# Performance work log

Measured on AMD Instinct MI355X. Metric: run time of the kernel, lower is better.

The kernel has to match this reference:

```python
import jax, jax.numpy as jnp
import numpy as np

N = 50000   # nodes
E = 600000  # edges
IN = 512    # in_channels
H = 128     # hidden_channels
B = 64      # graphs in batch
L = 4       # GatedGraphConv layers
VIEWS = [[0, 9, 10], [1, 2, 3], [4, 5, 6], [7, 8, 11, 12]]  # syntactic/sequential/semantic/discourse


def layer_norm(x, w, b, eps=1e-5):
    mu = x.mean(-1, keepdims=True)
    var = ((x - mu) ** 2).mean(-1, keepdims=True)
    return (x - mu) / jnp.sqrt(var + eps) * w + b


def setup_inputs() -> dict:
    key = jax.random.key(0)
    ks = jax.random.split(key, 32)
    p = lambda k, shape: (jax.random.normal(k, shape, jnp.float32) * 0.02)
    inp = {
        'x': jax.random.normal(ks[0], (N, IN), jnp.float32),
        'edge_index': jax.random.randint(ks[1], (2, E), 0, N, dtype=jnp.int32),
        'edge_type': jax.random.randint(ks[2], (E,), 0, 13, dtype=jnp.int32),
        'batch': jnp.sort(jax.random.randint(ks[3], (N,), 0, B, dtype=jnp.int32)),
        # input projection (Linear + LayerNorm)
        'proj_w': p(ks[4], (IN, H)), 'proj_b': p(ks[5], (H,)),
        'ln0_w': jnp.ones((H,), jnp.float32), 'ln0_b': jnp.zeros((H,), jnp.float32),
        # per-view GatedGraphConv: weight [views, layers, H, H] + GRUCell params [views, 3H, H]
        'ggnn_w': p(ks[6], (4, L, H, H)),
        'gru_wih': p(ks[7], (4, 3 * H, H)), 'gru_whh': p(ks[8], (4, 3 * H, H)),
        'gru_bih': p(ks[9], (4, 3 * H)), 'gru_bhh': p(ks[10], (4, 3 * H)),
        # per-view LayerNorm
        'vln_w': jnp.ones((4, H), jnp.float32), 'vln_b': jnp.zeros((4, H), jnp.float32),
        # attention fusion
        'q_w': p(ks[11], (H, H)), 'q_b': p(ks[12], (H,)),
        'k_w': p(ks[13], (H, H)), 'k_b': p(ks[14], (H,)),
        # classifier MLP: 2H -> H -> H//2 -> 1
        'c1_w': p(ks[15], (2 * H, H)), 'c1_b': p(ks[16], (H,)),
        'c2_w': p(ks[17], (H, H // 2)), 'c2_b': p(ks[18], (H // 2,)),
        'c3_w': p(ks[19], (H // 2, 1)), 'c3_b': p(ks[20], (1,)),
    }
    return inp


def reference(x, edge_index, edge_type, batch, proj_w, proj_b, ln0_w, ln0_b,
              ggnn_w, gru_wih, gru_whh, gru_bih, gru_bhh, vln_w, vln_b,
              q_w, q_b, k_w, k_b, c1_w, c1_b, c2_w, c2_b, c3_w, c3_b):
    # input projection: Linear -> LayerNorm -> GELU (dropout = identity in eval)
    h0 = jax.nn.gelu(layer_norm(x @ proj_w + proj_b, ln0_w, ln0_b), approximate=False)
    src, dst = edge_index[0], edge_index[1]
    views = []
    for v in range(4):
        emask = jnp.zeros((E,), bool)
        for t in VIEWS[v]:
            emask = emask | (edge_type == t)
        em = emask.astype(h0.dtype)[:, None]  # [E,1] edge-type view mask
        h = h0
        for i in range(L):
            m = h @ ggnn_w[v, i]                                   # [N,H]
            agg = jax.ops.segment_sum(m[src] * em, dst, num_segments=N)  # masked scatter-add
            # GRUCell(input=agg, hidden=h), torch gate order r,z,n
            gi = agg @ gru_wih[v].T + gru_bih[v]
            gh = h @ gru_whh[v].T + gru_bhh[v]
            ir, iz, inn = jnp.split(gi, 3, -1)
            hr, hz, hn = jnp.split(gh, 3, -1)
            r = jax.nn.sigmoid(ir + hr)
            z = jax.nn.sigmoid(iz + hz)
            n = jnp.tanh(inn + r * hn)
            h = (1.0 - z) * n + z * h
        views.append(layer_norm(h, vln_w[v], vln_b[v]) + h0)  # residual ViewEncoder
    hs = jnp.stack(views, 1)  # [N,4,H]
    # node-conditioned attention fusion
    q = jnp.tanh(h0 @ q_w + q_b)
    keys = hs @ k_w + k_b
    attn = jax.nn.softmax(jnp.einsum('nh,nvh->nv', q, keys) * (H ** -0.5), axis=-1)
    fused = jnp.einsum('nvh,nv->nh', hs, attn)
    # global mean + max pooling per graph
    cnt = jax.ops.segment_sum(jnp.ones((N,), fused.dtype), batch, num_segments=B)
    x_mean = jax.ops.segment_sum(fused, batch, num_segments=B) / jnp.maximum(cnt, 1.0)[:, None]
    x_max = jax.ops.segment_max(fused, batch, num_segments=B)
    g = jnp.concatenate([x_mean, x_max], -1)  # [B,2H]
    h1 = jax.nn.relu(g @ c1_w + c1_b)
    h2 = jax.nn.relu(h1 @ c2_w + c2_b)
    return h2 @ c3_w + c3_b  # [B,1] logits
```

## Files before the change

### kernel.cpp

```cpp
#include <hip/hip_runtime.h>
#include <math.h>


typedef __attribute__((ext_vector_type(8))) short short8;
typedef __attribute__((ext_vector_type(4))) float floatx4;

__device__ __forceinline__ unsigned short f2bf_rtn(float x) {
    unsigned u = __float_as_uint(x);
    return (unsigned short)((u + 0x7FFFu + ((u >> 16) & 1u)) >> 16);
}
__device__ __forceinline__ float bf2f(unsigned short h) {
    return __uint_as_float((unsigned)h << 16);
}
__device__ __forceinline__ float fsig(float x) {
    return __builtin_amdgcn_rcpf(1.0f + __expf(-x));
}
__device__ __forceinline__ float ftanh(float x) {
    return 1.0f - 2.0f * __builtin_amdgcn_rcpf(__expf(2.0f * x) + 1.0f);
}

__device__ __forceinline__ int view_of(int t) {
    return (t >= 1 && t <= 3) ? 1 : (t >= 4 && t <= 6) ? 2
         : ((t == 7) || (t == 8) || (t >= 11)) ? 3 : 0;
}

template <bool BT, int EPI>
__global__ __launch_bounds__(256, 2) void gemm_k(
    const float* __restrict__ A, const float* __restrict__ Bm,
    const float* __restrict__ bias, float* __restrict__ C,
    int N, int M, int K, long sA, long sB, long sC)
{
    __shared__ float As[32][132];
    __shared__ float Bs[32][132];
    A  += (long)blockIdx.z * sA;
    Bm += (long)blockIdx.z * sB;
    C  += (long)blockIdx.z * sC;
    const int r0 = blockIdx.x * 128;
    const int c0 = blockIdx.y * 128;
    const int tid = threadIdx.x;
    const int tx = tid & 15;
    const int ty = tid >> 4;

    float acc[8][8];
#pragma unroll
    for (int i = 0; i < 8; i++)
#pragma unroll
        for (int j = 0; j < 8; j++) acc[i][j] = 0.0f;

    for (int k0 = 0; k0 < K; k0 += 32) {
        {
            int arow = tid >> 3;
            int akq  = (tid & 7) << 2;
#pragma unroll
            for (int hh = 0; hh < 4; hh++) {
                int r  = arow + hh * 32;
                int gr = r0 + r;
                float4 av = make_float4(0.f, 0.f, 0.f, 0.f);
                if (gr < N) av = *(const float4*)(A + (long)gr * K + k0 + akq);
                As[akq + 0][r] = av.x; As[akq + 1][r] = av.y;
                As[akq + 2][r] = av.z; As[akq + 3][r] = av.w;
            }
        }
        if (BT) {
            int brow = tid >> 3;
            int bkq  = (tid & 7) << 2;
#pragma unroll
            for (int hh = 0; hh < 4; hh++) {
                int r = brow + hh * 32;
                float4 bv = *(const float4*)(Bm + (long)(c0 + r) * K + k0 + bkq);
                Bs[bkq + 0][r] = bv.x; Bs[bkq + 1][r] = bv.y;
                Bs[bkq + 2][r] = bv.z; Bs[bkq + 3][r] = bv.w;
            }
        } else {
            int kk0 = tid >> 5;
            int bmq = (tid & 31) << 2;
#pragma unroll
            for (int hh = 0; hh < 4; hh++) {
                int kk = kk0 + hh * 8;
                float4 bv = *(const float4*)(Bm + (long)(k0 + kk) * M + c0 + bmq);
                *(float4*)&Bs[kk][bmq] = bv;
            }
        }
        __syncthreads();
#pragma unroll
        for (int k = 0; k < 32; k++) {
            float4 a0 = *(const float4*)&As[k][ty << 2];
            float4 a1 = *(const float4*)&As[k][64 + (ty << 2)];
            float4 b0 = *(const float4*)&Bs[k][tx << 2];
            float4 b1 = *(const float4*)&Bs[k][64 + (tx << 2)];
            float av[8] = {a0.x, a0.y, a0.z, a0.w, a1.x, a1.y, a1.z, a1.w};
            float bv[8] = {b0.x, b0.y, b0.z, b0.w, b1.x, b1.y, b1.z, b1.w};
#pragma unroll
            for (int i = 0; i < 8; i++)
#pragma unroll
                for (int j = 0; j < 8; j++) acc[i][j] += av[i] * bv[j];
        }
        __syncthreads();
    }

    float bb[8] = {0, 0, 0, 0, 0, 0, 0, 0};
    if (bias) {
        float4 b0 = *(const float4*)(bias + c0 + (tx << 2));
        float4 b1 = *(const float4*)(bias + c0 + 64 + (tx << 2));
        bb[0] = b0.x; bb[1] = b0.y; bb[2] = b0.z; bb[3] = b0.w;
        bb[4] = b1.x; bb[5] = b1.y; bb[6] = b1.z; bb[7] = b1.w;
    }
#pragma unroll
    for (int i = 0; i < 8; i++) {
        int r = (i < 4) ? (r0 + (ty << 2) + i) : (r0 + 64 + (ty << 2) + i - 4);
        if (r < N) {
            float v[8];
#pragma unroll
            for (int j = 0; j < 8; j++) {
                v[j] = acc[i][j] + bb[j];
                if (EPI == 1) v[j] = tanhf(v[j]);
            }
            *(float4*)(C + (long)r * M + c0 + (tx << 2)) = make_float4(v[0], v[1], v[2], v[3]);
            *(float4*)(C + (long)r * M + c0 + 64 + (tx << 2)) = make_float4(v[4], v[5], v[6], v[7]);
        }
    }
}

__global__ __launch_bounds__(256) void build_p_k(
    const float* __restrict__ gwih, const float* __restrict__ gwhh,
    const float* __restrict__ gbih, const float* __restrict__ gbhh,
    float* __restrict__ pih, float* __restrict__ phh, float* __restrict__ bp)
{
    int idx = blockIdx.x * 256 + threadIdx.x;
    if (idx < 16 * 65536) {
        int z = idx >> 16, rem = idx & 65535;
        int k = rem >> 9, mcol = rem & 511;
        int ch = mcol >> 2, g = mcol & 3;
        int v = z >> 2;
        const float* Wih = gwih + (long)v * 384 * 128;
        float val = 0.0f;
        if (g == 0) val = Wih[ch * 128 + k];
        else if (g == 1) val = Wih[(128 + ch) * 128 + k];
        else if (g == 2) val = Wih[(256 + ch) * 128 + k];
        pih[idx] = val;
    }
    if (idx < 4 * 65536) {
        int v = idx >> 16, rem = idx & 65535;
        int k = rem >> 9, mcol = rem & 511;
        int ch = mcol >> 2, g = mcol & 3;
        const float* Whh = gwhh + (long)v * 384 * 128;
        float val = 0.0f;
        if (g == 0) val = Whh[ch * 128 + k];
        else if (g == 1) val = Whh[(128 + ch) * 128 + k];
        else if (g == 3) val = Whh[(256 + ch) * 128 + k];
        phh[idx] = val;
    }
    if (idx < 4 * 512) {
        int v = idx >> 9, mcol = idx & 511;
        int ch = mcol >> 2, g = mcol & 3;
        float val;
        if (g == 0) val = gbih[v * 384 + ch] + gbhh[v * 384 + ch];
        else if (g == 1) val = gbih[v * 384 + 128 + ch] + gbhh[v * 384 + 128 + ch];
        else if (g == 2) val = gbih[v * 384 + 256 + ch];
        else val = gbhh[v * 384 + 256 + ch];
        bp[idx] = val;
    }
}

__global__ __launch_bounds__(256) void pack_b_k(
    const float* __restrict__ wcomb, const float* __restrict__ phh,
    short* __restrict__ Bp)
{
    int idx = blockIdx.x * 256 + threadIdx.x;
    if (idx >= 16 * 256 * 512) return;
    int z = idx >> 17, rem = idx & 131071;
    int k = rem >> 9, col = rem & 511;
    int g  = col & 3;
    int q  = (col >> 2) & 3;
    int tn = (col >> 4) & 7;
    int ch = ((col >> 7) << 5) + (q << 3) + tn;
    int mcol = (ch << 2) + g;
    float val = (k < 128) ? wcomb[(long)z * 65536 + k * 512 + mcol]
                          : phh[(long)(z >> 2) * 65536 + (k - 128) * 512 + mcol];
    long dst = ((long)(z * 8 + (k >> 5)) * 512 + col) * 32 + ((k >> 3) & 3) * 8 + (k & 7);
    Bp[dst] = (short)f2bf_rtn(val);
}

template <bool BT>
__global__ __launch_bounds__(256) void pack_w_k(
    const float* __restrict__ W, short* __restrict__ bhi, short* __restrict__ blo, int K)
{
    int idx = blockIdx.x * 256 + threadIdx.x;
    if (idx >= K * 128) return;
    int k = idx >> 7, col = idx & 127;
    float v = BT ? W[col * K + k] : W[k * 128 + col];
    unsigned short h = f2bf_rtn(v);
    float fh = __uint_as_float((unsigned)h << 16);
    long dst = ((long)(k >> 5) * 128 + col) * 32 + ((k >> 3) & 3) * 8 + (k & 7);
    bhi[dst] = (short)h;
    blo[dst] = (short)f2bf_rtn(v - fh);
}

template <int EPI>
__global__ __launch_bounds__(256, 4) void gemm_mfma_k(
    const float* __restrict__ A, const short* __restrict__ Bhi,
    const short* __restrict__ Blo, const float* __restrict__ bias,
    float* __restrict__ C, int N, int K)
{
    __shared__ __align__(16) short Ahi[64 * 40];
    __shared__ __align__(16) short Alo[64 * 40];
    const int r0 = blockIdx.x * 64;
    const int tid = threadIdx.x;
    const int l = tid & 63, w = tid >> 6;
    const int wrow = w * 16;
    const int m = l & 15, q = l >> 4;

    floatx4 acc[8];
#pragma unroll
    for (int b = 0; b < 8; b++) acc[b] = (floatx4)0.0f;

    const int arow = tid >> 2;
    const int fcol = (tid & 3) * 8;
    const int gr = r0 + arow;
    const int nks = K >> 5;

    for (int ks = 0; ks < nks; ks++) {
        float xv[8];
        if (gr < N) {
            float4 x0 = *(const float4*)(A + (long)gr * K + ks * 32 + fcol);
            float4 x1 = *(const float4*)(A + (long)gr * K + ks * 32 + fcol + 4);
            xv[0] = x0.x; xv[1] = x0.y; xv[2] = x0.z; xv[3] = x0.w;
            xv[4] = x1.x; xv[5] = x1.y; xv[6] = x1.z; xv[7] = x1.w;
        } else {
#pragma unroll
            for (int u = 0; u < 8; u++) xv[u] = 0.0f;
        }
        short8 vhi, vlo;
#pragma unroll
        for (int u = 0; u < 8; u++) {
            unsigned short hb = f2bf_rtn(xv[u]);
            float fh = __uint_as_float((unsigned)hb << 16);
            vhi[u] = (short)hb;
            vlo[u] = (short)f2bf_rtn(xv[u] - fh);
        }
        *(short8*)&Ahi[arow * 40 + fcol] = vhi;
        *(short8*)&Alo[arow * 40 + fcol] = vlo;
        __syncthreads();
        short8 ah = *(short8*)&Ahi[(wrow + m) * 40 + q * 8];
        short8 al = *(short8*)&Alo[(wrow + m) * 40 + q * 8];
#pragma unroll
        for (int tn = 0; tn < 8; tn++) {
            int col = tn * 16 + m;
            short8 bh = *(const short8*)(Bhi + ((long)ks * 128 + col) * 32 + q * 8);
            short8 bl = *(const short8*)(Blo + ((long)ks * 128 + col) * 32 + q * 8);
            acc[tn] = __builtin_amdgcn_mfma_f32_16x16x32_bf16(ah, bh, acc[tn], 0, 0, 0);
            acc[tn] = __builtin_amdgcn_mfma_f32_16x16x32_bf16(al, bh, acc[tn], 0, 0, 0);
            acc[tn] = __builtin_amdgcn_mfma_f32_16x16x32_bf16(ah, bl, acc[tn], 0, 0, 0);
        }
        __syncthreads();
    }

#pragma unroll
    for (int tn = 0; tn < 8; tn++) {
        int col = tn * 16 + m;
        float bb = bias ? bias[col] : 0.0f;
#pragma unroll
        for (int reg = 0; reg < 4; reg++) {
            int row = r0 + wrow + q * 4 + reg;
            if (row < N) {
                float v = acc[tn][reg] + bb;
                if (EPI == 1) v = ftanh(v);
                C[(long)row * 128 + col] = v;
            }
        }
    }
}

__global__ __launch_bounds__(256, 4) void gemm_gru_mfma_k(
    const short* __restrict__ hb, const short* __restrict__ hpHi,
    const short* __restrict__ hpLo, const short* __restrict__ Bp,
    const float* __restrict__ bp, short* __restrict__ outHi,
    short* __restrict__ outLo, const int* __restrict__ off,
    const int* __restrict__ esrc, int N, long sV, long sHb, long sHp)
{
    __shared__ __align__(16) short As[8 * 64 * 40];
    const int xb = blockIdx.x;
    const int x = (xb & 7) | ((xb >> 4) << 3);
    const int yb = (xb >> 3) & 1;
    if (x * 64 >= N) return;
    const int z = blockIdx.z;
    const short* hbz = hb + (long)z * sHb;
    const short* hph = hpHi + (long)z * sHp;
    const short* hpl = hpLo + (long)z * sHp;
    Bp  += (long)z * 524288;
    bp  += (long)z * 512;
    outHi += (long)z * sV;
    outLo += (long)z * sV;
    const int r0  = x * 64;
    const int c0b = yb * 256;
    const int tid = threadIdx.x;
    const int l = tid & 63, w = tid >> 6;
    const int wrow = (w & 1) * 32, wcol = (w >> 1) * 128;
    const int m = l & 15, q = l >> 4;

    const int arow = tid >> 2;
    const int fcol = (tid & 3) * 8;
    const int gr = r0 + arow;

    {
        const int cg = tid & 3;
        float accS[32];
#pragma unroll
        for (int u = 0; u < 32; u++) accS[u] = 0.0f;
        if (gr < N) {
            const int idx = z * N + gr;
            int j = off[idx];
            const int end = off[idx + 1];
            if (j < end) {
                const short* sp = hb + (long)esrc[j] * 128 + (cg << 5);
                short8 p0 = *(const short8*)(sp);
                short8 p1 = *(const short8*)(sp + 8);
                short8 p2 = *(const short8*)(sp + 16);
                short8 p3 = *(const short8*)(sp + 24);
                for (; j < end;) {
                    short8 c0 = p0, c1 = p1, c2 = p2, c3 = p3;
                    ++j;
                    if (j < end) {
                        const short* sq = hb + (long)esrc[j] * 128 + (cg << 5);
                        p0 = *(const short8*)(sq);
                        p1 = *(const short8*)(sq + 8);
                        p2 = *(const short8*)(sq + 16);
                        p3 = *(const short8*)(sq + 24);
                    }
#pragma unroll
                    for (int u = 0; u < 8; u++) {
                        accS[u]      += bf2f((unsigned short)c0[u]);
                        accS[8 + u]  += bf2f((unsigned short)c1[u]);
                        accS[16 + u] += bf2f((unsigned short)c2[u]);
                        accS[24 + u] += bf2f((unsigned short)c3[u]);
                    }
                }
            }
        }
#pragma unroll
        for (int ub = 0; ub < 4; ub++) {
            short8 o;
#pragma unroll
            for (int u = 0; u < 8; u++) o[u] = (short)f2bf_rtn(accS[ub * 8 + u]);
            *(short8*)&As[cg * 2560 + arow * 40 + ub * 8] = o;
        }
    }

#pragma unroll
    for (int ks2 = 0; ks2 < 4; ks2++) {
        short8 av = (short8)0;
        if (gr < N) av = *(const short8*)(hbz + (long)gr * 128 + ks2 * 32 + fcol);
        *(short8*)&As[(4 + ks2) * 2560 + arow * 40 + fcol] = av;
    }
    __syncthreads();

    floatx4 acc[2][8];
#pragma unroll
    for (int a = 0; a < 2; a++)
#pragma unroll
        for (int b = 0; b < 8; b++) acc[a][b] = (floatx4)0.0f;

#pragma unroll
    for (int ks = 0; ks < 8; ks++) {
        short8 bfr[8];
#pragma unroll
        for (int tn = 0; tn < 8; tn++) {
            int col = c0b + wcol + tn * 16 + m;
            bfr[tn] = *(const short8*)(Bp + ((long)ks * 512 + col) * 32 + q * 8);
        }
        short8 a0 = *(short8*)&As[ks * 2560 + (wrow + m) * 40 + q * 8];
        short8 a1 = *(short8*)&As[ks * 2560 + (wrow + 16 + m) * 40 + q * 8];
#pragma unroll
        for (int tn = 0; tn < 8; tn++) {
            acc[0][tn] = __builtin_amdgcn_mfma_f32_16x16x32_bf16(bfr[tn], a0, acc[0][tn], 0, 0, 0);
            acc[1][tn] = __builtin_amdgcn_mfma_f32_16x16x32_bf16(bfr[tn], a1, acc[1][tn], 0, 0, 0);
        }
    }

    const int chq = ((c0b + wcol) >> 2) + q * 8;
#pragma unroll
    for (int a = 0; a < 2; a++) {
        const int row = r0 + wrow + a * 16 + m;
        if (row < N) {
            short8 h8 = *(const short8*)(hph + (long)row * 128 + chq);
            short8 l8 = *(const short8*)(hpl + (long)row * 128 + chq);
            float hnv[8];
            short8 ohi, olo;
#pragma unroll
            for (int tn = 0; tn < 8; tn++) {
                float hp = bf2f((unsigned short)h8[tn]) + bf2f((unsigned short)l8[tn]);
                float4 bv = *(const float4*)(bp + (chq + tn) * 4);
                floatx4 A = acc[a][tn];
                float rr = fsig(A[0] + bv.x);
                float zz = fsig(A[1] + bv.y);
                float nn = ftanh(A[2] + bv.z + rr * (A[3] + bv.w));
                hnv[tn] = (1.0f - zz) * nn + zz * hp;
                unsigned short hh = f2bf_rtn(hnv[tn]);
                ohi[tn] = (short)hh;
                olo[tn] = (short)f2bf_rtn(hnv[tn] - bf2f(hh));
            }
            *(short8*)(outHi + (long)row * 128 + chq) = ohi;
            *(short8*)(outLo + (long)row * 128 + chq) = olo;
        }
    }
}

__global__ __launch_bounds__(256) void ln_gelu_k(
    float* __restrict__ h0, short* __restrict__ h0b, short* __restrict__ h0lo,
    const float* __restrict__ w, const float* __restrict__ b, int N)
{
    long t = (long)blockIdx.x * 256 + threadIdx.x;
    int n = (int)(t >> 5), lane = (int)(t & 31);
    if (n >= N) return;
    float* p = h0 + (long)n * 128 + lane * 4;
    float4 x = *(float4*)p;
    float s = x.x + x.y + x.z + x.w;
#pragma unroll
    for (int off = 16; off >= 1; off >>= 1) s += __shfl_xor(s, off);
    float mu = s * (1.0f / 128.0f);
    float4 d = make_float4(x.x - mu, x.y - mu, x.z - mu, x.w - mu);
    float ss = d.x * d.x + d.y * d.y + d.z * d.z + d.w * d.w;
#pragma unroll
    for (int off = 16; off >= 1; off >>= 1) ss += __shfl_xor(ss, off);
    float inv = 1.0f / sqrtf(ss * (1.0f / 128.0f) + 1e-5f);
    float4 wv = *(const float4*)(w + lane * 4);
    float4 bv = *(const float4*)(b + lane * 4);
    float y[4] = {d.x * inv * wv.x + bv.x, d.y * inv * wv.y + bv.y,
                  d.z * inv * wv.z + bv.z, d.w * inv * wv.w + bv.w};
#pragma unroll
    for (int i = 0; i < 4; i++)
        y[i] = 0.5f * y[i] * (1.0f + erff(y[i] * 0.70710678118654752f));
    *(float4*)p = make_float4(y[0], y[1], y[2], y[3]);
    ushort4 hb, lb;
    hb.x = f2bf_rtn(y[0]); lb.x = f2bf_rtn(y[0] - bf2f(hb.x));
    hb.y = f2bf_rtn(y[1]); lb.y = f2bf_rtn(y[1] - bf2f(hb.y));
    hb.z = f2bf_rtn(y[2]); lb.z = f2bf_rtn(y[2] - bf2f(hb.z));
    hb.w = f2bf_rtn(y[3]); lb.w = f2bf_rtn(y[3] - bf2f(hb.w));
    *(ushort4*)(h0b + (long)n * 128 + lane * 4) = hb;
    *(ushort4*)(h0lo + (long)n * 128 + lane * 4) = lb;
}

__global__ __launch_bounds__(256) void count_k(
    const int* __restrict__ dst, const int* __restrict__ et,
    int* __restrict__ cnt, int E, int N)
{
    int e = blockIdx.x * 256 + threadIdx.x;
    if (e >= E) return;
    int v = view_of(et[e]);
    atomicAdd(&cnt[v * N + dst[e]], 1);
}

__global__ __launch_bounds__(256) void scan1_k(
    const int* __restrict__ cnt, int* __restrict__ off, int* __restrict__ bsum, int n)
{
    __shared__ int sm[256];
    int base = blockIdx.x * 1024;
    int tid = threadIdx.x;
    int v[4]; int s = 0;
#pragma unroll
    for (int i = 0; i < 4; i++) {
        int idx = base + tid * 4 + i;
        v[i] = (idx < n) ? cnt[idx] : 0; s += v[i];
    }
    sm[tid] = s; __syncthreads();
    for (int o = 1; o < 256; o <<= 1) {
        int t2 = (tid >= o) ? sm[tid - o] : 0;
        __syncthreads(); sm[tid] += t2; __syncthreads();
    }
    int run = sm[tid] - s;
    if (tid == 255) bsum[blockIdx.x] = sm[255];
#pragma unroll
    for (int i = 0; i < 4; i++) {
        int idx = base + tid * 4 + i;
        if (idx < n) off[idx] = run;
        run += v[i];
    }
}

__global__ __launch_bounds__(256) void scan2_k(int* __restrict__ bsum, int nb)
{
    __shared__ int sm[256];
    int tid = threadIdx.x;
    int v = (tid < nb) ? bsum[tid] : 0;
    sm[tid] = v; __syncthreads();
    for (int o = 1; o < 256; o <<= 1) {
        int t2 = (tid >= o) ? sm[tid - o] : 0;
        __syncthreads(); sm[tid] += t2; __syncthreads();
    }
    if (tid < nb) bsum[tid] = sm[tid] - v;
}

__global__ __launch_bounds__(256) void scan3_k(
    int* __restrict__ off, int* __restrict__ cursor,
    const int* __restrict__ bsum, int n, int total)
{
    int i = blockIdx.x * 256 + threadIdx.x;
    if (i < n) {
        int o = off[i] + bsum[i >> 10];
        off[i] = o; cursor[i] = o;
    }
    if (i == 0) off[n] = total;
}

__global__ __launch_bounds__(256) void fill_k(
    const int* __restrict__ src, const int* __restrict__ dst,
    const int* __restrict__ et, int* __restrict__ cursor,
    int* __restrict__ esrc, int* __restrict__ esrc0, int E, int N)
{
    int e = blockIdx.x * 256 + threadIdx.x;
    if (e >= E) return;
    int v = view_of(et[e]);
    int b = v * N + dst[e];
    int pos = atomicAdd(&cursor[b], 1);
    esrc[pos] = v * N + src[e];
    esrc0[pos] = src[e];
}

__global__ __launch_bounds__(256) void fusion_k(
    const short* __restrict__ hi, const short* __restrict__ lo,
    const float* __restrict__ h0, const float* __restrict__ q,
    const float* __restrict__ u, const float* __restrict__ kb,
    const float* __restrict__ vw, const float* __restrict__ vb,
    float* __restrict__ fused, int N)
{
    long t = (long)blockIdx.x * 256 + threadIdx.x;
    int n = (int)(t >> 5), lane = (int)(t & 31);
    if (n >= N) return;
    float4 qv = *(const float4*)(q + (long)n * 128 + lane * 4);
    float4 kv = *(const float4*)(kb + lane * 4);
    float4 uv = *(const float4*)(u + (long)n * 128 + lane * 4);
    float4 h0v = *(const float4*)(h0 + (long)n * 128 + lane * 4);
    float part = qv.x * kv.x + qv.y * kv.y + qv.z * kv.z + qv.w * kv.w;
    float hs[4][4];
    float lg[4];
#pragma unroll
    for (int v = 0; v < 4; v++) {
        long base = ((long)v * N + n) * 128 + lane * 4;
        ushort4 hu = *(const ushort4*)(hi + base);
        ushort4 lu = *(const ushort4*)(lo + base);
        float hv0 = bf2f(hu.x) + bf2f(lu.x);
        float hv1 = bf2f(hu.y) + bf2f(lu.y);
        float hv2 = bf2f(hu.z) + bf2f(lu.z);
        float hv3 = bf2f(hu.w) + bf2f(lu.w);
        float s = hv0 + hv1 + hv2 + hv3;
#pragma unroll
        for (int off = 16; off >= 1; off >>= 1) s += __shfl_xor(s, off);
        float mu = s * (1.0f / 128.0f);
        float d0 = hv0 - mu, d1 = hv1 - mu, d2 = hv2 - mu, d3 = hv3 - mu;
        float ss = d0 * d0 + d1 * d1 + d2 * d2 + d3 * d3;
#pragma unroll
        for (int off = 16; off >= 1; off >>= 1) ss += __shfl_xor(ss, off);
        float inv = 1.0f / sqrtf(ss * (1.0f / 128.0f) + 1e-5f);
        float4 wv = *(const float4*)(vw + v * 128 + lane * 4);
        float4 bv = *(const float4*)(vb + v * 128 + lane * 4);
        hs[v][0] = d0 * inv * wv.x + bv.x + h0v.x;
        hs[v][1] = d1 * inv * wv.y + bv.y + h0v.y;
        hs[v][2] = d2 * inv * wv.z + bv.z + h0v.z;
        hs[v][3] = d3 * inv * wv.w + bv.w + h0v.w;
        lg[v] = hs[v][0] * uv.x + hs[v][1] * uv.y + hs[v][2] * uv.z + hs[v][3] * uv.w;
    }
#pragma unroll
    for (int off = 16; off >= 1; off >>= 1) {
        part += __shfl_xor(part, off);
#pragma unroll
        for (int v = 0; v < 4; v++) lg[v] += __shfl_xor(lg[v], off);
    }
    const float scale = 0.08838834764831845f;
    float mx = -1e30f;
#pragma unroll
    for (int v = 0; v < 4; v++) { lg[v] = (lg[v] + part) * scale; mx = fmaxf(mx, lg[v]); }
    float se = 0.0f;
#pragma unroll
    for (int v = 0; v < 4; v++) { lg[v] = expf(lg[v] - mx); se += lg[v]; }
    float inv = 1.0f / se;
    float4 f = make_float4(0.f, 0.f, 0.f, 0.f);
#pragma unroll
    for (int v = 0; v < 4; v++) {
        float a = lg[v] * inv;
        f.x += a * hs[v][0]; f.y += a * hs[v][1];
        f.z += a * hs[v][2]; f.w += a * hs[v][3];
    }
    *(float4*)(fused + (long)n * 128 + lane * 4) = f;
}

__global__ __launch_bounds__(256) void pool_k(
    const float* __restrict__ fused, const int* __restrict__ batch,
    float* __restrict__ meanb, float* __restrict__ maxb, int N)
{
    __shared__ float s_sum[256], s_max[256];
    int b = blockIdx.x;
    int lo = 0, hi = N;
    while (lo < hi) { int mid = (lo + hi) >> 1; if (batch[mid] < b) lo = mid + 1; else hi = mid; }
    int beg = lo;
    lo = beg; hi = N;
    while (lo < hi) { int mid = (lo + hi) >> 1; if (batch[mid] < b + 1) lo = mid + 1; else hi = mid; }
    int end = lo;
    int tid = threadIdx.x;
    int c = tid & 127, half = tid >> 7;
    float sum = 0.0f, mx = __int_as_float(0xff800000);
    for (int n = beg + half; n < end; n += 2) {
        float v = fused[(long)n * 128 + c];
        sum += v; mx = fmaxf(mx, v);
    }
    s_sum[tid] = sum; s_max[tid] = mx;
    __syncthreads();
    if (half == 0) {
        float tot = s_sum[tid] + s_sum[tid + 128];
        float m2 = fmaxf(s_max[tid], s_max[tid + 128]);
        int cnt = end - beg;
        meanb[b * 128 + c] = tot / (float)max(cnt, 1);
        maxb[b * 128 + c] = m2;
    }
}

__global__ __launch_bounds__(256) void classifier_k(
    const float* __restrict__ meanb, const float* __restrict__ maxb,
    const float* __restrict__ c1w, const float* __restrict__ c1b,
    const float* __restrict__ c2w, const float* __restrict__ c2b,
    const float* __restrict__ c3w, const float* __restrict__ c3b,
    float* __restrict__ out)
{
    __shared__ float g[256];
    __shared__ float h1[128];
    __shared__ float h2[64];
    int b = blockIdx.x, tid = threadIdx.x;
    g[tid] = (tid < 128) ? meanb[b * 128 + tid] : maxb[b * 128 + (tid - 128)];
    __syncthreads();
    if (tid < 128) {
        float acc = c1b[tid];
        for (int k = 0; k < 256; k++) acc += g[k] * c1w[k * 128 + tid];
        h1[tid] = fmaxf(acc, 0.0f);
    }
    __syncthreads();
    if (tid < 64) {
        float acc = c2b[tid];
        for (int k = 0; k < 128; k++) acc += h1[k] * c2w[k * 64 + tid];
        h2[tid] = fmaxf(acc, 0.0f);
    }
    __syncthreads();
    if (tid < 64) {
        float p = h2[tid] * c3w[tid];
#pragma unroll
        for (int off = 32; off >= 1; off >>= 1) p += __shfl_xor(p, off);
        if (tid == 0) out[b] = c3b[0] + p;
    }
}

extern "C" void kernel_launch(void* const* d_in, const int* in_sizes, int n_in,
                              void* d_out, int out_size, void* d_ws, size_t ws_size,
                              hipStream_t stream) {
    (void)n_in; (void)out_size; (void)ws_size;
    const float* x      = (const float*)d_in[0];
    const int*   eidx   = (const int*)d_in[1];
    const int*   etype  = (const int*)d_in[2];
    const int*   batch  = (const int*)d_in[3];
    const float* proj_w = (const float*)d_in[4];
    const float* proj_b = (const float*)d_in[5];
    const float* ln0_w  = (const float*)d_in[6];
    const float* ln0_b  = (const float*)d_in[7];
    const float* ggnn_w = (const float*)d_in[8];
    const float* gwih   = (const float*)d_in[9];
    const float* gwhh   = (const float*)d_in[10];
    const float* gbih   = (const float*)d_in[11];
    const float* gbhh   = (const float*)d_in[12];
    const float* vln_w  = (const float*)d_in[13];
    const float* vln_b  = (const float*)d_in[14];
    const float* q_w    = (const float*)d_in[15];
    const float* q_b    = (const float*)d_in[16];
    const float* k_w    = (const float*)d_in[17];
    const float* k_b    = (const float*)d_in[18];
    const float* c1w    = (const float*)d_in[19];
    const float* c1b    = (const float*)d_in[20];
    const float* c2w    = (const float*)d_in[21];
    const float* c2b    = (const float*)d_in[22];
    const float* c3w    = (const float*)d_in[23];
    const float* c3b    = (const float*)d_in[24];
    float* out = (float*)d_out;

    const int N = in_sizes[3];
    const int E = in_sizes[2];
    const int IN = in_sizes[0] / N;
    const int H = 128, L = 4;
    const int N4 = 4 * N;

    long NH = (long)N * H;
    float* ws = (float*)d_ws;
    float* h0 = ws;
    float* hfz = h0 + NH;
    short* loA = (short*)hfz;
    short* loB = loA + 4 * NH;
    float* poolMean = hfz + 4 * NH;
    float* poolMax  = poolMean + 8192;
    float* bp = poolMax + 8192;
    short* h0b = (short*)(bp + 2048);
    short* hiA = h0b + NH;
    short* hiB = hiA + 4 * NH;
    short* Sb  = hiB + 4 * NH;
    short* Bp  = Sb + 4 * NH;
    short* prjHi = Bp + 16 * 131072;
    short* prjLo = prjHi + 65536;
    short* qwHi  = prjLo + 65536;
    short* qwLo  = qwHi + 16384;
    short* kwHi  = qwLo + 16384;
    short* kwLo  = kwHi + 16384;
    int* iOff  = (int*)(kwLo + 16384);
    int* iCnt  = iOff + N4 + 1;
    int* iCur  = iCnt + N4;
    int* iBsum = iCur + N4;
    int* iEsrc  = iBsum + 256;
    int* iEsrc0 = iEsrc + E;
    float* wcomb = hfz;
    float* pih   = hfz + 16 * 65536;
    float* phh   = pih + 16 * 65536;
    short* lo0 = loB;
    float* qbuf  = (float*)Sb;
    float* ubuf  = qbuf + NH;
    float* fused = (float*)hiA;

    int rb = (int)(((long)N * 32 + 255) / 256);
    int eb = (E + 255) / 256;
    int nbScan = (N4 + 1023) / 1024;
    int gx64 = (N + 63) / 64;
    int gxp = ((gx64 + 7) / 8) * 8;

    const int* esrc_in = eidx;
    const int* edst_in = eidx + E;

    hipMemsetAsync(iCnt, 0, (size_t)N4 * sizeof(int), stream);
    count_k<<<eb, 256, 0, stream>>>(edst_in, etype, iCnt, E, N);
    scan1_k<<<nbScan, 256, 0, stream>>>(iCnt, iOff, iBsum, N4);
    scan2_k<<<1, 256, 0, stream>>>(iBsum, nbScan);
    scan3_k<<<(N4 + 255) / 256, 256, 0, stream>>>(iOff, iCur, iBsum, N4, E);
    fill_k<<<eb, 256, 0, stream>>>(esrc_in, edst_in, etype, iCur, iEsrc, iEsrc0, E, N);

    build_p_k<<<(16 * 65536 + 255) / 256, 256, 0, stream>>>(
        gwih, gwhh, gbih, gbhh, pih, phh, bp);
    gemm_k<false, 0><<<dim3(1, 4, 16), 256, 0, stream>>>(
        ggnn_w, pih, nullptr, wcomb, 128, 512, 128,
        (long)H * H, 65536, 65536);
    pack_b_k<<<(16 * 256 * 512 + 255) / 256, 256, 0, stream>>>(wcomb, phh, Bp);
    pack_w_k<false><<<(IN * 128 + 255) / 256, 256, 0, stream>>>(proj_w, prjHi, prjLo, IN);
    pack_w_k<false><<<(128 * 128 + 255) / 256, 256, 0, stream>>>(q_w, qwHi, qwLo, 128);
    pack_w_k<true><<<(128 * 128 + 255) / 256, 256, 0, stream>>>(k_w, kwHi, kwLo, 128);

    gemm_mfma_k<0><<<gx64, 256, 0, stream>>>(x, prjHi, prjLo, proj_b, h0, N, IN);
    ln_gelu_k<<<rb, 256, 0, stream>>>(h0, h0b, lo0, ln0_w, ln0_b, N);

    const short* hin = h0b;  long sHb = 0;
    const short* hpH = h0b;  const short* hpL = lo0;  long sHp = 0;
    short* oHi = hiA; short* oLo = loA;
    for (int i = 0; i < L; i++) {
        const int* es = (i == 0) ? iEsrc0 : iEsrc;
        gemm_gru_mfma_k<<<dim3(2 * gxp, 1, 4), 256, 0, stream>>>(
            hin, hpH, hpL, Bp + (long)i * 131072, bp, oHi, oLo, iOff, es,
            N, NH, sHb, sHp);
        hpH = oHi; hpL = oLo; sHp = NH;
        hin = oHi; sHb = NH;
        if (oHi == hiA) { oHi = hiB; oLo = loB; }
        else            { oHi = hiA; oLo = loA; }
    }

    gemm_mfma_k<1><<<gx64, 256, 0, stream>>>(h0, qwHi, qwLo, q_b, qbuf, N, 128);
    gemm_mfma_k<0><<<gx64, 256, 0, stream>>>(qbuf, kwHi, kwLo, nullptr, ubuf, N, 128);
    fusion_k<<<rb, 256, 0, stream>>>(hiB, loB, h0, qbuf, ubuf, k_b,
                                     vln_w, vln_b, fused, N);
    pool_k<<<64, 256, 0, stream>>>(fused, batch, poolMean, poolMax, N);
    classifier_k<<<64, 256, 0, stream>>>(
        poolMean, poolMax, c1w, c1b, c2w, c2b, c3w, c3b, out);
}
```

Measured before the change: 1.286 ms.

## Merge GRU gemm column halves into one 512-thread block per row tile

The fused gather+GEMM+GRU kernel previously launched two 256-thread blocks per 64-row tile, one for each half of the 512 gate columns, and each block repeated the neighbour aggregation for the same rows. Now a single 512-thread block covers all 512 columns: eight waves tile the output, and the gather is spread over eight threads per row with half the accumulator registers each. This removes the duplicated irregular gather work and the swizzled block indexing. In exchange, launch bounds move to 512 threads with a higher occupancy target, which tightens the per-thread register budget for the MFMA accumulators and may cause spills.

New measurement: 2.167 ms. +68.5%, slower.

```diff
diff --git a/kernel.cpp b/kernel.cpp
--- a/kernel.cpp
+++ b/kernel.cpp
@@ -271,7 +271,7 @@
     }
 }
 
-__global__ __launch_bounds__(256, 4) void gemm_gru_mfma_k(
+__global__ __launch_bounds__(512, 6) void gemm_gru_mfma_k(
     const short* __restrict__ hb, const short* __restrict__ hpHi,
     const short* __restrict__ hpLo, const short* __restrict__ Bp,
     const float* __restrict__ bp, short* __restrict__ outHi,
@@ -279,10 +279,7 @@
     const int* __restrict__ esrc, int N, long sV, long sHb, long sHp)
 {
     __shared__ __align__(16) short As[8 * 64 * 40];
-    const int xb = blockIdx.x;
-    const int x = (xb & 7) | ((xb >> 4) << 3);
-    const int yb = (xb >> 3) & 1;
-    if (x * 64 >= N) return;
+    const int x = blockIdx.x;
     const int z = blockIdx.z;
     const short* hbz = hb + (long)z * sHb;
     const short* hph = hpHi + (long)z * sHp;
@@ -292,65 +289,64 @@
     outHi += (long)z * sV;
     outLo += (long)z * sV;
     const int r0  = x * 64;
-    const int c0b = yb * 256;
     const int tid = threadIdx.x;
     const int l = tid & 63, w = tid >> 6;
     const int wrow = (w & 1) * 32, wcol = (w >> 1) * 128;
     const int m = l & 15, q = l >> 4;
 
-    const int arow = tid >> 2;
-    const int fcol = (tid & 3) * 8;
-    const int gr = r0 + arow;
+    const int row8 = tid >> 3;
+    const int cg8  = tid & 7;
+    const int gr = r0 + row8;
 
     {
-        const int cg = tid & 3;
-        float accS[32];
-#pragma unroll
-        for (int u = 0; u < 32; u++) accS[u] = 0.0f;
+        float accS[16];
+#pragma unroll
+        for (int u = 0; u < 16; u++) accS[u] = 0.0f;
         if (gr < N) {
             const int idx = z * N + gr;
             int j = off[idx];
             const int end = off[idx + 1];
             if (j < end) {
-                const short* sp = hb + (long)esrc[j] * 128 + (cg << 5);
+                const short* sp = hb + (long)esrc[j] * 128 + (cg8 << 4);
                 short8 p0 = *(const short8*)(sp);
                 short8 p1 = *(const short8*)(sp + 8);
-                short8 p2 = *(const short8*)(sp + 16);
-                short8 p3 = *(const short8*)(sp + 24);
                 for (; j < end;) {
-                    short8 c0 = p0, c1 = p1, c2 = p2, c3 = p3;
+                    short8 c0 = p0, c1 = p1;
                     ++j;
                     if (j < end) {
-                        const short* sq = hb + (long)esrc[j] * 128 + (cg << 5);
+                        const short* sq = hb + (long)esrc[j] * 128 + (cg8 << 4);
                         p0 = *(const short8*)(sq);
                         p1 = *(const short8*)(sq + 8);
-                        p2 = *(const short8*)(sq + 16);
-                        p3 = *(const short8*)(sq + 24);
                     }
 #pragma unroll
                     for (int u = 0; u < 8; u++) {
-                        accS[u]      += bf2f((unsigned short)c0[u]);
-                        accS[8 + u]  += bf2f((unsigned short)c1[u]);
-                        accS[16 + u] += bf2f((unsigned short)c2[u]);
-                        accS[24 + u] += bf2f((unsigned short)c3[u]);
+                        accS[u]     += bf2f((unsigned short)c0[u]);
+                        accS[8 + u] += bf2f((unsigned short)c1[u]);
                     }
                 }
             }
         }
-#pragma unroll
-        for (int ub = 0; ub < 4; ub++) {
-            short8 o;
-#pragma unroll
-            for (int u = 0; u < 8; u++) o[u] = (short)f2bf_rtn(accS[ub * 8 + u]);
-            *(short8*)&As[cg * 2560 + arow * 40 + ub * 8] = o;
-        }
-    }
-
-#pragma unroll
-    for (int ks2 = 0; ks2 < 4; ks2++) {
-        short8 av = (short8)0;
-        if (gr < N) av = *(const short8*)(hbz + (long)gr * 128 + ks2 * 32 + fcol);
-        *(short8*)&As[(4 + ks2) * 2560 + arow * 40 + fcol] = av;
+        short8 o0, o1;
+#pragma unroll
+        for (int u = 0; u < 8; u++) {
+            o0[u] = (short)f2bf_rtn(accS[u]);
+            o1[u] = (short)f2bf_rtn(accS[8 + u]);
+        }
+        const int base = (cg8 >> 1) * 2560 + row8 * 40 + (cg8 & 1) * 16;
+        *(short8*)&As[base]     = o0;
+        *(short8*)&As[base + 8] = o1;
+    }
+
+    {
+        short8 h0v = (short8)0, h1v = (short8)0;
+        if (gr < N) {
+            const short* hp = hbz + (long)gr * 128 + (cg8 << 4);
+            h0v = *(const short8*)(hp);
+            h1v = *(const short8*)(hp + 8);
+        }
+        const int base = (4 + (cg8 >> 1)) * 2560 + row8 * 40 + (cg8 & 1) * 16;
+        *(short8*)&As[base]     = h0v;
+        *(short8*)&As[base + 8] = h1v;
     }
     __syncthreads();
 
@@ -365,7 +361,7 @@
         short8 bfr[8];
 #pragma unroll
         for (int tn = 0; tn < 8; tn++) {
-            int col = c0b + wcol + tn * 16 + m;
+            int col = wcol + tn * 16 + m;
             bfr[tn] = *(const short8*)(Bp + ((long)ks * 512 + col) * 32 + q * 8);
         }
         short8 a0 = *(short8*)&As[ks * 2560 + (wrow + m) * 40 + q * 8];
@@ -377,7 +373,7 @@
         }
     }
 
-    const int chq = ((c0b + wcol) >> 2) + q * 8;
+    const int chq = (wcol >> 2) + q * 8;
 #pragma unroll
     for (int a = 0; a < 2; a++) {
         const int row = r0 + wrow + a * 16 + m;
@@ -721,7 +717,6 @@
     int eb = (E + 255) / 256;
     int nbScan = (N4 + 1023) / 1024;
     int gx64 = (N + 63) / 64;
-    int gxp = ((gx64 + 7) / 8) * 8;
 
     const int* esrc_in = eidx;
     const int* edst_in = eidx + E;
@@ -751,7 +746,7 @@
     short* oHi = hiA; short* oLo = loA;
     for (int i = 0; i < L; i++) {
         const int* es = (i == 0) ? iEsrc0 : iEsrc;
-        gemm_gru_mfma_k<<<dim3(2 * gxp, 1, 4), 256, 0, stream>>>(
+        gemm_gru_mfma_k<<<dim3(gx64, 1, 4), 512, 0, stream>>>(
             hin, hpH, hpL, Bp + (long)i * 131072, bp, oHi, oLo, iOff, es,
             N, NH, sHb, sHp);
         hpH = oHi; hpL = oLo; sHp = NH;
```
